# Kernel tuning notes

Hardware: AMD Instinct MI355X
Metric: run time of the kernel (lower is better)

## Reference

```python
import jax, jax.numpy as jnp
import numpy as np

NUM_LEVELS = 16
LEVEL_DIM = 2
BASE_RES = 16
MAX_RES = 2048
HASHMAP_SIZE = 1 << 19
N_POINTS = 2000000

# Instant-NGP geometric progression of grid resolutions
_scale = np.exp2(np.log2(MAX_RES / BASE_RES) / (NUM_LEVELS - 1))
RESOLUTIONS = [int(np.ceil(BASE_RES * _scale ** l)) for l in range(NUM_LEVELS)]

# corner offsets of the unit cube, shape [8, 3]
_OFFS = np.stack(np.meshgrid([0, 1], [0, 1], [0, 1], indexing='ij'), -1).reshape(8, 3)
_PRIMES = np.array([1, 2654435761, 805459861], dtype=np.uint32)


def grid_encode(x, table):
    """x: [N,3] in [0,1]; table: [L, T, F] -> [N, L*F]."""
    offs = jnp.asarray(_OFFS, dtype=jnp.int32)          # [8,3]
    feats = []
    for l, res in enumerate(RESOLUTIONS):
        pos = x * (res - 1)                              # [N,3]
        pos_i = jnp.clip(jnp.floor(pos).astype(jnp.int32), 0, res - 2)
        frac = pos - pos_i.astype(pos.dtype)             # [N,3]
        corners = pos_i[:, None, :] + offs[None]         # [N,8,3]
        if res ** 3 <= HASHMAP_SIZE:
            # dense (collision-free) indexing for coarse levels
            idx = corners[..., 0] + res * (corners[..., 1] + res * corners[..., 2])
        else:
            # spatial hash: xor of coordinate * prime, mod table size
            c = corners.astype(jnp.uint32)
            h = (c[..., 0] * _PRIMES[0]) ^ (c[..., 1] * _PRIMES[1]) ^ (c[..., 2] * _PRIMES[2])
            idx = (h % jnp.uint32(HASHMAP_SIZE)).astype(jnp.int32)
        vals = table[l][idx]                             # [N,8,F] gather
        # multilinear interpolation weights per corner
        w = jnp.prod(jnp.where(offs[None].astype(bool), frac[:, None, :], 1.0 - frac[:, None, :]), axis=-1)  # [N,8]
        feats.append(jnp.einsum('nc,ncf->nf', w, vals))
    return jnp.concatenate(feats, axis=-1)               # [N, 32]


def setup_inputs() -> dict:
    key = jax.random.key(0)
    ks = jax.random.split(key, 6)
    x = jax.random.uniform(ks[0], (N_POINTS, 3), dtype=jnp.float32)
    table = jax.random.uniform(ks[1], (NUM_LEVELS, HASHMAP_SIZE, LEVEL_DIM),
                               dtype=jnp.float32, minval=-1e-4, maxval=1e-4)
    in_dim = NUM_LEVELS * LEVEL_DIM  # 32
    W1 = jax.random.normal(ks[2], (in_dim, 64), dtype=jnp.float32) / np.sqrt(in_dim)
    W2 = jax.random.normal(ks[3], (64, 64), dtype=jnp.float32) / 8.0
    W3 = jax.random.normal(ks[4], (64, 64), dtype=jnp.float32) / 8.0
    Wo = jax.random.normal(ks[5], (64, 1), dtype=jnp.float32) / 8.0
    z = lambda n: jnp.zeros((n,), dtype=jnp.float32)
    return {"x": x, "table": table, "W1": W1, "b1": z(64), "W2": W2, "b2": z(64),
            "W3": W3, "b3": z(64), "Wo": Wo, "bo": z(1)}


def reference(x, table, W1, b1, W2, b2, W3, b3, Wo, bo):
    h = grid_encode(x, table)                 # [N,32]
    h = jax.nn.relu(h @ W1 + b1)
    h = jax.nn.relu(h @ W2 + b2)
    h = jax.nn.relu(h @ W3 + b3)
    return h @ Wo + bo                        # [N,1]
```

## Files before the change

### kernel.cpp

```cpp
#include <hip/hip_runtime.h>
#include <cmath>
#include <cstdint>


#define HASH_SZ (1u << 19)
#define HMASK   (HASH_SZ - 1u)
#define PR2 2654435761u
#define PR3 805459861u

typedef float v2f __attribute__((ext_vector_type(2)));
typedef float v4f __attribute__((ext_vector_type(4)));
typedef v4f v4fu __attribute__((aligned(8)));
typedef v2f v2fu __attribute__((aligned(8)));
typedef short bf16x8 __attribute__((ext_vector_type(8)));
typedef float f32x4 __attribute__((ext_vector_type(4)));

struct ResArr { int r[16]; };

__device__ __forceinline__ unsigned short bf16_rne(float f) {
    union { float f; unsigned u; } v; v.f = f;
    unsigned u = v.u;
    unsigned r = (u + 0x7fffu + ((u >> 16) & 1u)) >> 16;
    return (unsigned short)r;
}
__device__ __forceinline__ float bf16f(unsigned short h) {
    union { unsigned u; float f; } v; v.u = ((unsigned)h) << 16;
    return v.f;
}
__device__ __forceinline__ void split8(const float* x, bf16x8& hi, bf16x8& lo) {
    #pragma unroll
    for (int j = 0; j < 8; ++j) {
        union { float f; unsigned u; } v; v.f = x[j];
        const unsigned hu = v.u & 0xffff0000u;
        hi[j] = (short)(hu >> 16);
        union { unsigned u; float f; } hf; hf.u = hu;
        const float d = x[j] - hf.f;
        union { float f; unsigned u; } dv; dv.f = d;
        lo[j] = (short)((dv.u + 0x7fffu + ((dv.u >> 16) & 1u)) >> 16);
    }
}

__device__ __forceinline__ void gather_one(
    const v2f* __restrict__ tbl, int res, bool dense,
    float px, float py, float pz, float& A0, float& A1)
{
    const float rf = (float)(res - 1);
    const float fx = px * rf, fy = py * rf, fz = pz * rf;
    int ix = (int)floorf(fx), iy = (int)floorf(fy), iz = (int)floorf(fz);
    ix = min(max(ix, 0), res - 2);
    iy = min(max(iy, 0), res - 2);
    iz = min(max(iz, 0), res - 2);
    const float tx = fx - (float)ix, ty = fy - (float)iy, tz = fz - (float)iz;
    const float sx = 1.f - tx, sy = 1.f - ty, sz = 1.f - tz;
    float a0 = 0.f, a1 = 0.f;

    if (dense) {
        const int b0 = ix + res * (iy + res * iz);
        v4fu P[4];
        #pragma unroll
        for (int c = 0; c < 4; ++c) {
            const int dy = c >> 1, dz = c & 1;
            P[c] = *(const v4fu*)((const float*)tbl + 2 * (b0 + res * dy + res * res * dz));
        }
        #pragma unroll
        for (int c = 0; c < 4; ++c) {
            const int dy = c >> 1, dz = c & 1;
            const float wyz = (dy ? ty : sy) * (dz ? tz : sz);
            const float w0 = sx * wyz, w1 = tx * wyz;
            a0 = fmaf(w0, P[c].x, a0); a1 = fmaf(w0, P[c].y, a1);
            a0 = fmaf(w1, P[c].z, a0); a1 = fmaf(w1, P[c].w, a1);
        }
    } else {
        uint32_t i0[4], i1[4];
        v4f P[4];
        #pragma unroll
        for (int c = 0; c < 4; ++c) {
            const int dy = c >> 1, dz = c & 1;
            const uint32_t r = (uint32_t)(iy + dy) * PR2 ^ (uint32_t)(iz + dz) * PR3;
            i0[c] = ((uint32_t)ix ^ r) & HMASK;
            i1[c] = ((uint32_t)(ix + 1) ^ r) & HMASK;
            P[c] = *(const v4f*)((const float*)tbl + 2 * (i0[c] & ~1u));
        }
        const bool odd = (ix & 1);
        v2f O[4];
        if (odd) {
            #pragma unroll
            for (int c = 0; c < 4; ++c) O[c] = tbl[i1[c]];
        } else {
            #pragma unroll
            for (int c = 0; c < 4; ++c) { v2f z = {0.f, 0.f}; O[c] = z; }
        }
        #pragma unroll
        for (int c = 0; c < 4; ++c) {
            const int dy = c >> 1, dz = c & 1;
            const bool hi = (i0[c] & 1);
            v2f c0, e;
            c0.x = hi ? P[c].z : P[c].x;  c0.y = hi ? P[c].w : P[c].y;
            e.x  = hi ? P[c].x : P[c].z;  e.y  = hi ? P[c].y : P[c].w;
            const v2f c1 = odd ? O[c] : e;
            const float wyz = (dy ? ty : sy) * (dz ? tz : sz);
            const float w0 = sx * wyz, w1 = tx * wyz;
            a0 = fmaf(w0, c0.x, a0); a1 = fmaf(w0, c0.y, a1);
            a0 = fmaf(w1, c1.x, a0); a1 = fmaf(w1, c1.y, a1);
        }
    }
    A0 = a0; A1 = a1;
}

template<int NLEV>
__global__ __launch_bounds__(256, 8)
void encode_k(const float* __restrict__ x, const float* __restrict__ table,
              v2f* __restrict__ featT, int n, int lb, ResArr rv)
{
    const int nth2 = gridDim.x * 512;
    for (int q = (blockIdx.x * 256 + threadIdx.x) * 2; q < n; q += nth2) {
        float p0x, p0y, p0z, p1x, p1y, p1z;
        const bool two = (q + 1 < n);
        if (two) {
            const v4fu a = __builtin_nontemporal_load((const v4fu*)(x + 3 * q));
            const v2f  b = __builtin_nontemporal_load((const v2fu*)(x + 3 * q + 4));
            p0x = a.x; p0y = a.y; p0z = a.z; p1x = a.w; p1y = b.x; p1z = b.y;
        } else {
            p0x = x[3 * q]; p0y = x[3 * q + 1]; p0z = x[3 * q + 2];
            p1x = p0x; p1y = p0y; p1z = p0z;
        }
        #pragma unroll
        for (int il = 0; il < NLEV; ++il) {
            const int l = lb + il;
            const int res = rv.r[l];
            const bool dense = ((long long)res * res * res <= (long long)HASH_SZ);
            const v2f* tbl = (const v2f*)table + (size_t)l * HASH_SZ;
            float a00, a01, a10, a11;
            gather_one(tbl, res, dense, p0x, p0y, p0z, a00, a01);
            gather_one(tbl, res, dense, p1x, p1y, p1z, a10, a11);
            if (two) {
                v4f st; st.x = a00; st.y = a01; st.z = a10; st.w = a11;
                __builtin_nontemporal_store(st, (v4f*)&featT[(size_t)l * n + q]);
            } else {
                v2f st; st.x = a00; st.y = a01;
                __builtin_nontemporal_store(st, &featT[(size_t)l * n + q]);
            }
        }
    }
}

__global__ void prep_weights(const float* __restrict__ W1,
                             const float* __restrict__ W2,
                             const float* __restrict__ W3,
                             unsigned short* __restrict__ wb)
{
    const int tid = threadIdx.x;
    const int nb = tid >> 6, lane = tid & 63;
    const int l15 = lane & 15, q = lane >> 4;
    #pragma unroll
    for (int j = 0; j < 8; ++j) {
        const float v = W1[(q * 8 + j) * 64 + nb * 16 + l15];
        const unsigned short h = bf16_rne(v);
        wb[(nb * 64 + lane) * 8 + j] = h;
        wb[2048 + (nb * 64 + lane) * 8 + j] = bf16_rne(v - bf16f(h));
    }
    #pragma unroll
    for (int kb = 0; kb < 2; ++kb) {
        #pragma unroll
        for (int j = 0; j < 8; ++j) {
            const int row = kb * 32 + q * 8 + j;
            const int idx = ((kb * 4 + nb) * 64 + lane) * 8 + j;
            float v = W2[row * 64 + nb * 16 + l15];
            unsigned short h = bf16_rne(v);
            wb[4096 + idx] = h;
            wb[8192 + idx] = bf16_rne(v - bf16f(h));
            v = W3[row * 64 + nb * 16 + l15];
            h = bf16_rne(v);
            wb[12288 + idx] = h;
            wb[16384 + idx] = bf16_rne(v - bf16f(h));
        }
    }
}

#define TSTR 65

__global__ __launch_bounds__(256, 4)
void mlp_mfma(const v2f* __restrict__ featT,
              const unsigned short* __restrict__ wb,
              const float* __restrict__ b1, const float* __restrict__ b2,
              const float* __restrict__ b3,
              const float* __restrict__ Wo, const float* __restrict__ bo,
              float* __restrict__ out, int n)
{
    __shared__ float sact[4][32 * TSTR];
    const int wave = threadIdx.x >> 6;
    const int lane = threadIdx.x & 63;
    const int l15 = lane & 15, quad = lane >> 4;
    const int p0 = (blockIdx.x * 4 + wave) * 32;
    if (p0 >= n) return;

    bf16x8 ah[2], al[2];
    #pragma unroll
    for (int t = 0; t < 2; ++t) {
        const int p = p0 + t * 16 + l15;
        const int pl = (p < n) ? p : (n - 1);
        float xv[8];
        #pragma unroll
        for (int jj = 0; jj < 4; ++jj) {
            const v2f f = featT[(size_t)(quad * 4 + jj) * n + pl];
            xv[2 * jj] = f.x; xv[2 * jj + 1] = f.y;
        }
        split8(xv, ah[t], al[t]);
    }

    f32x4 acc[2][4];
    #pragma unroll
    for (int nb = 0; nb < 4; ++nb) {
        const bf16x8 wh = *(const bf16x8*)(wb + (nb * 64 + lane) * 8);
        const bf16x8 wl = *(const bf16x8*)(wb + 2048 + (nb * 64 + lane) * 8);
        const float bv = b1[nb * 16 + l15];
        #pragma unroll
        for (int t = 0; t < 2; ++t) {
            f32x4 c = {bv, bv, bv, bv};
            c = __builtin_amdgcn_mfma_f32_16x16x32_bf16(ah[t], wl, c, 0, 0, 0);
            c = __builtin_amdgcn_mfma_f32_16x16x32_bf16(al[t], wh, c, 0, 0, 0);
            c = __builtin_amdgcn_mfma_f32_16x16x32_bf16(ah[t], wh, c, 0, 0, 0);
            acc[t][nb] = c;
        }
    }

    #pragma unroll
    for (int layer = 0; layer < 2; ++layer) {
        #pragma unroll
        for (int t = 0; t < 2; ++t)
            #pragma unroll
            for (int nb = 0; nb < 4; ++nb)
                #pragma unroll
                for (int r = 0; r < 4; ++r)
                    sact[wave][(t * 16 + quad * 4 + r) * TSTR + nb * 16 + l15] =
                        fmaxf(acc[t][nb][r], 0.f);

        bf16x8 a2h[2][2], a2l[2][2];
        #pragma unroll
        for (int t = 0; t < 2; ++t) {
            float x2[16];
            #pragma unroll
            for (int kb = 0; kb < 2; ++kb)
                #pragma unroll
                for (int j = 0; j < 8; ++j)
                    x2[kb * 8 + j] =
                        sact[wave][(t * 16 + l15) * TSTR + kb * 32 + quad * 8 + j];
            split8(x2,     a2h[t][0], a2l[t][0]);
            split8(x2 + 8, a2h[t][1], a2l[t][1]);
        }

        const int base_h = layer ? 12288 : 4096;
        const int base_l = layer ? 16384 : 8192;
        const float* __restrict__ bias = layer ? b3 : b2;
        #pragma unroll
        for (int nb = 0; nb < 4; ++nb) {
            const float bv = bias[nb * 16 + l15];
            f32x4 c[2];
            #pragma unroll
            for (int t = 0; t < 2; ++t) { f32x4 z = {bv, bv, bv, bv}; c[t] = z; }
            #pragma unroll
            for (int kb = 0; kb < 2; ++kb) {
                const int idx = ((kb * 4 + nb) * 64 + lane) * 8;
                const bf16x8 wh = *(const bf16x8*)(wb + base_h + idx);
                const bf16x8 wl = *(const bf16x8*)(wb + base_l + idx);
                #pragma unroll
                for (int t = 0; t < 2; ++t) {
                    c[t] = __builtin_amdgcn_mfma_f32_16x16x32_bf16(a2h[t][kb], wl, c[t], 0, 0, 0);
                    c[t] = __builtin_amdgcn_mfma_f32_16x16x32_bf16(a2l[t][kb], wh, c[t], 0, 0, 0);
                    c[t] = __builtin_amdgcn_mfma_f32_16x16x32_bf16(a2h[t][kb], wh, c[t], 0, 0, 0);
                }
            }
            #pragma unroll
            for (int t = 0; t < 2; ++t) acc[t][nb] = c[t];
        }
    }

    const float wo = Wo[0 * 16 + l15];
    (void)wo;
    float part[2][4];
    #pragma unroll
    for (int t = 0; t < 2; ++t)
        #pragma unroll
        for (int r = 0; r < 4; ++r) {
            float s = 0.f;
            #pragma unroll
            for (int nb = 0; nb < 4; ++nb)
                s = fmaf(fmaxf(acc[t][nb][r], 0.f), Wo[nb * 16 + l15], s);
            part[t][r] = s;
        }
    #pragma unroll
    for (int mask = 1; mask < 16; mask <<= 1)
        #pragma unroll
        for (int t = 0; t < 2; ++t)
            #pragma unroll
            for (int r = 0; r < 4; ++r)
                part[t][r] += __shfl_xor(part[t][r], mask, 64);

    if (l15 == 0) {
        const float b = bo[0];
        #pragma unroll
        for (int t = 0; t < 2; ++t)
            #pragma unroll
            for (int r = 0; r < 4; ++r) {
                const int po = p0 + t * 16 + quad * 4 + r;
                if (po < n) out[po] = part[t][r] + b;
            }
    }
}

__global__ __launch_bounds__(256, 3)
void mlp_forward(const v2f* __restrict__ featT,
                 const float* __restrict__ W1, const float* __restrict__ b1,
                 const float* __restrict__ W2, const float* __restrict__ b2,
                 const float* __restrict__ W3, const float* __restrict__ b3,
                 const float* __restrict__ Wo, const float* __restrict__ bo,
                 float* __restrict__ out, int n)
{
    const int p = blockIdx.x * 256 + threadIdx.x;
    if (p >= n) return;
    const v2f z2 = {0.f, 0.f};
    v2f A[32], B[32];
    #pragma unroll
    for (int jq = 0; jq < 16; ++jq) {
        const v4f b = *(const v4f*)(b1 + 4 * jq);
        A[2 * jq] = b.xy; A[2 * jq + 1] = b.zw;
    }
    #pragma unroll
    for (int l = 0; l < 16; ++l) {
        const v2f f = __builtin_nontemporal_load(&featT[(size_t)l * n + p]);
        const v4f* w0 = (const v4f*)(W1 + (size_t)(2 * l) * 64);
        const v4f* w1 = (const v4f*)(W1 + (size_t)(2 * l + 1) * 64);
        const v2f h0 = {f.x, f.x}, h1 = {f.y, f.y};
        #pragma unroll
        for (int jq = 0; jq < 16; ++jq) {
            const v4f wa = w0[jq];
            A[2 * jq]     = __builtin_elementwise_fma(h0, wa.xy, A[2 * jq]);
            A[2 * jq + 1] = __builtin_elementwise_fma(h0, wa.zw, A[2 * jq + 1]);
        }
        #pragma unroll
        for (int jq = 0; jq < 16; ++jq) {
            const v4f wb2 = w1[jq];
            A[2 * jq]     = __builtin_elementwise_fma(h1, wb2.xy, A[2 * jq]);
            A[2 * jq + 1] = __builtin_elementwise_fma(h1, wb2.zw, A[2 * jq + 1]);
        }
    }
    #pragma unroll
    for (int j = 0; j < 32; ++j) A[j] = __builtin_elementwise_max(A[j], z2);
    #pragma unroll
    for (int jq = 0; jq < 16; ++jq) {
        const v4f b = *(const v4f*)(b2 + 4 * jq);
        B[2 * jq] = b.xy; B[2 * jq + 1] = b.zw;
    }
    #pragma unroll
    for (int k = 0; k < 64; ++k) {
        const float hv = A[k >> 1][k & 1];
        const v2f h = {hv, hv};
        const v4f* w = (const v4f*)(W2 + (size_t)k * 64);
        #pragma unroll
        for (int jq = 0; jq < 16; ++jq) {
            const v4f wa = w[jq];
            B[2 * jq]     = __builtin_elementwise_fma(h, wa.xy, B[2 * jq]);
            B[2 * jq + 1] = __builtin_elementwise_fma(h, wa.zw, B[2 * jq + 1]);
        }
    }
    #pragma unroll
    for (int j = 0; j < 32; ++j) B[j] = __builtin_elementwise_max(B[j], z2);
    #pragma unroll
    for (int jq = 0; jq < 16; ++jq) {
        const v4f b = *(const v4f*)(b3 + 4 * jq);
        A[2 * jq] = b.xy; A[2 * jq + 1] = b.zw;
    }
    #pragma unroll
    for (int k = 0; k < 64; ++k) {
        const float hv = B[k >> 1][k & 1];
        const v2f h = {hv, hv};
        const v4f* w = (const v4f*)(W3 + (size_t)k * 64);
        #pragma unroll
        for (int jq = 0; jq < 16; ++jq) {
            const v4f wa = w[jq];
            A[2 * jq]     = __builtin_elementwise_fma(h, wa.xy, A[2 * jq]);
            A[2 * jq + 1] = __builtin_elementwise_fma(h, wa.zw, A[2 * jq + 1]);
        }
    }
    v2f o2 = z2;
    #pragma unroll
    for (int jq = 0; jq < 16; ++jq) {
        const v4f wa = *(const v4f*)(Wo + 4 * jq);
        o2 = __builtin_elementwise_fma(__builtin_elementwise_max(A[2 * jq], z2),     wa.xy, o2);
        o2 = __builtin_elementwise_fma(__builtin_elementwise_max(A[2 * jq + 1], z2), wa.zw, o2);
    }
    out[p] = o2.x + o2.y + bo[0];
}

__global__ __launch_bounds__(256, 2)
void hashpinn_fused(const float* __restrict__ x,
                    const float* __restrict__ table,
                    const float* __restrict__ W1, const float* __restrict__ b1,
                    const float* __restrict__ W2, const float* __restrict__ b2,
                    const float* __restrict__ W3, const float* __restrict__ b3,
                    const float* __restrict__ Wo, const float* __restrict__ bo,
                    float* __restrict__ out, int n, ResArr rv)
{
    const int p = blockIdx.x * 256 + threadIdx.x;
    if (p >= n) return;
    const float px = x[3*p+0], py = x[3*p+1], pz = x[3*p+2];
    float feat[32];
    #pragma unroll
    for (int l = 0; l < 16; ++l) {
        const int res = rv.r[l];
        const float rf = (float)(res - 1);
        const float fx = px*rf, fy = py*rf, fz = pz*rf;
        int ix=(int)floorf(fx), iy=(int)floorf(fy), iz=(int)floorf(fz);
        ix=min(max(ix,0),res-2); iy=min(max(iy,0),res-2); iz=min(max(iz,0),res-2);
        const float tx=fx-(float)ix, ty=fy-(float)iy, tz=fz-(float)iz;
        const float sx=1.f-tx, sy=1.f-ty, sz=1.f-tz;
        const float2* tbl=(const float2*)table+(size_t)l*HASH_SZ;
        const bool dense=((long long)res*res*res<=(long long)HASH_SZ);
        float a0=0.f, a1=0.f;
        #pragma unroll
        for (int c=0;c<8;++c){
            const uint32_t cx=(uint32_t)(ix+((c>>2)&1));
            const uint32_t cy=(uint32_t)(iy+((c>>1)&1));
            const uint32_t cz=(uint32_t)(iz+(c&1));
            uint32_t idx = dense ? cx+(uint32_t)res*(cy+(uint32_t)res*cz)
                                 : ((cx*1u ^ cy*PR2 ^ cz*PR3)&HMASK);
            const float2 v=tbl[idx];
            const float w=(((c>>2)&1)?tx:sx)*(((c>>1)&1)?ty:sy)*((c&1)?tz:sz);
            a0=fmaf(w,v.x,a0); a1=fmaf(w,v.y,a1);
        }
        feat[2*l]=a0; feat[2*l+1]=a1;
    }
    float A[64], B[64];
    #pragma unroll
    for (int j=0;j<64;++j) A[j]=b1[j];
    #pragma unroll
    for (int k=0;k<32;++k){ const float h=feat[k];
        #pragma unroll
        for (int j=0;j<64;++j) A[j]=fmaf(h,W1[k*64+j],A[j]); }
    #pragma unroll 1
    for (int it=0;it<2;++it){
        const float* W = it?W3:W2; const float* bb = it?b3:b2;
        #pragma unroll
        for (int j=0;j<64;++j){ A[j]=fmaxf(A[j],0.f); B[j]=bb[j]; }
        #pragma unroll
        for (int k=0;k<64;++k){ const float h=A[k];
            #pragma unroll
            for (int j=0;j<64;++j) B[j]=fmaf(h,W[k*64+j],B[j]); }
        #pragma unroll
        for (int j=0;j<64;++j) A[j]=B[j];
    }
    float o=bo[0];
    #pragma unroll
    for (int j=0;j<64;++j) o=fmaf(fmaxf(A[j],0.f),Wo[j],o);
    out[p]=o;
}

static inline void launch_encode(int nlev, const float* x, const float* table,
                                 v2f* featT, int n, int lb, const ResArr& rv,
                                 hipStream_t stream) {
    const dim3 g(4096), b(256);
    switch (nlev) {
        case 1: hipLaunchKernelGGL(encode_k<1>, g, b, 0, stream, x, table, featT, n, lb, rv); break;
        case 2: hipLaunchKernelGGL(encode_k<2>, g, b, 0, stream, x, table, featT, n, lb, rv); break;
        case 3: hipLaunchKernelGGL(encode_k<3>, g, b, 0, stream, x, table, featT, n, lb, rv); break;
        case 4: hipLaunchKernelGGL(encode_k<4>, g, b, 0, stream, x, table, featT, n, lb, rv); break;
        case 5: hipLaunchKernelGGL(encode_k<5>, g, b, 0, stream, x, table, featT, n, lb, rv); break;
        case 6: hipLaunchKernelGGL(encode_k<6>, g, b, 0, stream, x, table, featT, n, lb, rv); break;
        case 7: hipLaunchKernelGGL(encode_k<7>, g, b, 0, stream, x, table, featT, n, lb, rv); break;
        default: hipLaunchKernelGGL(encode_k<8>, g, b, 0, stream, x, table, featT, n, lb, rv); break;
    }
}

extern "C" void kernel_launch(void* const* d_in, const int* in_sizes, int n_in,
                              void* d_out, int out_size, void* d_ws, size_t ws_size,
                              hipStream_t stream) {
    const float* x     = (const float*)d_in[0];
    const float* table = (const float*)d_in[1];
    const float* W1    = (const float*)d_in[2];
    const float* b1    = (const float*)d_in[3];
    const float* W2    = (const float*)d_in[4];
    const float* b2    = (const float*)d_in[5];
    const float* W3    = (const float*)d_in[6];
    const float* b3    = (const float*)d_in[7];
    const float* Wo    = (const float*)d_in[8];
    const float* bo    = (const float*)d_in[9];
    float* out = (float*)d_out;

    const int n = in_sizes[0] / 3;

    ResArr rv;
    const double scale = std::exp2(std::log2(2048.0 / 16.0) / 15.0);
    for (int l = 0; l < 16; ++l)
        rv.r[l] = (int)std::ceil(16.0 * std::pow(scale, (double)l));

    int dense_end = 0;
    while (dense_end < 16) {
        long long r = rv.r[dense_end];
        if (r * r * r <= (long long)HASH_SZ) ++dense_end; else break;
    }
    if (dense_end > 8) dense_end = 8;

    const size_t feat_bytes = (size_t)n * 16 * sizeof(v2f);
    const size_t wb_bytes = 20480 * sizeof(unsigned short);

    if (ws_size >= feat_bytes + wb_bytes) {
        v2f* featT = (v2f*)d_ws;
        unsigned short* wb = (unsigned short*)((char*)d_ws + feat_bytes);

        hipLaunchKernelGGL(prep_weights, dim3(1), dim3(256), 0, stream, W1, W2, W3, wb);

        if (dense_end > 0)
            launch_encode(dense_end, x, table, featT, n, 0, rv, stream);
        for (int l = dense_end; l < 16; ++l)
            launch_encode(1, x, table, featT, n, l, rv, stream);

        const int nblocks = (n + 127) / 128;
        hipLaunchKernelGGL(mlp_mfma, dim3(nblocks), dim3(256), 0, stream,
                           featT, wb, b1, b2, b3, Wo, bo, out, n);
    } else if (ws_size >= feat_bytes) {
        v2f* featT = (v2f*)d_ws;
        if (dense_end > 0)
            launch_encode(dense_end, x, table, featT, n, 0, rv, stream);
        for (int l = dense_end; l < 16; ++l)
            launch_encode(1, x, table, featT, n, l, rv, stream);
        hipLaunchKernelGGL(mlp_forward, dim3((n + 255) / 256), dim3(256), 0, stream,
                           featT, W1, b1, W2, b2, W3, b3, Wo, bo, out, n);
    } else {
        hipLaunchKernelGGL(hashpinn_fused, dim3((n + 255) / 256), dim3(256), 0, stream,
                           x, table, W1, b1, W2, b2, W3, b3, Wo, bo, out, n, rv);
    }
}
```

Before: 1.082 ms.

## Pre-split features to bf16 hi/lo in encoder and swap MLP activations via shuffles

The encoder now stores each feature pair as packed bf16 hi/lo words instead of fp32, so the MLP kernel loads ready-made MFMA operands without splitting them. The MFMA operand order is swapped (weights as A, activations as B), which lets inter-layer activations be redistributed with wave shuffles instead of a per-wave LDS transpose buffer. Bias and output-weight loads become vectorized, and the final reduction needs fewer shuffles. Dropping the LDS buffer allows a higher occupancy bound, at the cost of extra shuffle and select instructions and a fallback path that now decodes the packed format.

After: 1.133 ms. 1.05x slower.

```diff
diff --git a/kernel.cpp b/kernel.cpp
--- a/kernel.cpp
+++ b/kernel.cpp
@@ -14,6 +14,9 @@
 typedef v2f v2fu __attribute__((aligned(8)));
 typedef short bf16x8 __attribute__((ext_vector_type(8)));
 typedef float f32x4 __attribute__((ext_vector_type(4)));
+typedef unsigned int u32;
+typedef u32 u32x2 __attribute__((ext_vector_type(2)));
+typedef u32 u32x4 __attribute__((ext_vector_type(4)));
 
 struct ResArr { int r[16]; };
 
@@ -38,6 +41,19 @@
         union { float f; unsigned u; } dv; dv.f = d;
         lo[j] = (short)((dv.u + 0x7fffu + ((dv.u >> 16) & 1u)) >> 16);
     }
+}
+__device__ __forceinline__ u32 rne16u(float f) {
+    union { float f; u32 u; } v; v.f = f;
+    return (v.u + 0x7fffu + ((v.u >> 16) & 1u)) >> 16;
+}
+__device__ __forceinline__ u32x2 pack_split2(float f0, float f1) {
+    union { float f; u32 u; } a, b; a.f = f0; b.f = f1;
+    const u32 h0 = a.u & 0xffff0000u, h1 = b.u & 0xffff0000u;
+    union { u32 u; float f; } ha, hb; ha.u = h0; hb.u = h1;
+    u32x2 r;
+    r.x = (h0 >> 16) | h1;
+    r.y = rne16u(f0 - ha.f) | (rne16u(f1 - hb.f) << 16);
+    return r;
 }
 
 __device__ __forceinline__ void gather_one(
@@ -110,7 +126,7 @@
 template<int NLEV>
 __global__ __launch_bounds__(256, 8)
 void encode_k(const float* __restrict__ x, const float* __restrict__ table,
-              v2f* __restrict__ featT, int n, int lb, ResArr rv)
+              u32x2* __restrict__ featT, int n, int lb, ResArr rv)
 {
     const int nth2 = gridDim.x * 512;
     for (int q = (blockIdx.x * 256 + threadIdx.x) * 2; q < n; q += nth2) {
@@ -134,11 +150,13 @@
             gather_one(tbl, res, dense, p0x, p0y, p0z, a00, a01);
             gather_one(tbl, res, dense, p1x, p1y, p1z, a10, a11);
             if (two) {
-                v4f st; st.x = a00; st.y = a01; st.z = a10; st.w = a11;
-                __builtin_nontemporal_store(st, (v4f*)&featT[(size_t)l * n + q]);
+                const u32x2 e0 = pack_split2(a00, a01);
+                const u32x2 e1 = pack_split2(a10, a11);
+                u32x4 st; st.x = e0.x; st.y = e0.y; st.z = e1.x; st.w = e1.y;
+                __builtin_nontemporal_store(st, (u32x4*)&featT[(size_t)l * n + q]);
             } else {
-                v2f st; st.x = a00; st.y = a01;
-                __builtin_nontemporal_store(st, &featT[(size_t)l * n + q]);
+                __builtin_nontemporal_store(pack_split2(a00, a01),
+                                            &featT[(size_t)l * n + q]);
             }
         }
     }
@@ -177,35 +195,37 @@
     }
 }
 
-#define TSTR 65
-
-__global__ __launch_bounds__(256, 4)
-void mlp_mfma(const v2f* __restrict__ featT,
+__global__ __launch_bounds__(256, 6)
+void mlp_mfma(const u32x2* __restrict__ featT,
               const unsigned short* __restrict__ wb,
               const float* __restrict__ b1, const float* __restrict__ b2,
               const float* __restrict__ b3,
               const float* __restrict__ Wo, const float* __restrict__ bo,
               float* __restrict__ out, int n)
 {
-    __shared__ float sact[4][32 * TSTR];
     const int wave = threadIdx.x >> 6;
     const int lane = threadIdx.x & 63;
     const int l15 = lane & 15, quad = lane >> 4;
     const int p0 = (blockIdx.x * 4 + wave) * 32;
     if (p0 >= n) return;
 
-    bf16x8 ah[2], al[2];
+    const int s0 = (((2 * quad) & 3) << 4) + l15;
+    const int s1 = (((2 * quad + 1) & 3) << 4) + l15;
+    const bool hiHalf = (quad >= 2);
+
+    bf16x8 bh[2], bl[2];
     #pragma unroll
     for (int t = 0; t < 2; ++t) {
         const int p = p0 + t * 16 + l15;
         const int pl = (p < n) ? p : (n - 1);
-        float xv[8];
+        u32x4 hw, lw;
         #pragma unroll
         for (int jj = 0; jj < 4; ++jj) {
-            const v2f f = featT[(size_t)(quad * 4 + jj) * n + pl];
-            xv[2 * jj] = f.x; xv[2 * jj + 1] = f.y;
-        }
-        split8(xv, ah[t], al[t]);
+            const u32x2 v = featT[(size_t)(quad * 4 + jj) * n + pl];
+            hw[jj] = v.x; lw[jj] = v.y;
+        }
+        bh[t] = *(bf16x8*)&hw;
+        bl[t] = *(bf16x8*)&lw;
     }
 
     f32x4 acc[2][4];
@@ -213,51 +233,46 @@
     for (int nb = 0; nb < 4; ++nb) {
         const bf16x8 wh = *(const bf16x8*)(wb + (nb * 64 + lane) * 8);
         const bf16x8 wl = *(const bf16x8*)(wb + 2048 + (nb * 64 + lane) * 8);
-        const float bv = b1[nb * 16 + l15];
+        const f32x4 bv = *(const f32x4*)(b1 + nb * 16 + quad * 4);
         #pragma unroll
         for (int t = 0; t < 2; ++t) {
-            f32x4 c = {bv, bv, bv, bv};
-            c = __builtin_amdgcn_mfma_f32_16x16x32_bf16(ah[t], wl, c, 0, 0, 0);
-            c = __builtin_amdgcn_mfma_f32_16x16x32_bf16(al[t], wh, c, 0, 0, 0);
-            c = __builtin_amdgcn_mfma_f32_16x16x32_bf16(ah[t], wh, c, 0, 0, 0);
+            f32x4 c = bv;
+            c = __builtin_amdgcn_mfma_f32_16x16x32_bf16(wh, bl[t], c, 0, 0, 0);
+            c = __builtin_amdgcn_mfma_f32_16x16x32_bf16(wl, bh[t], c, 0, 0, 0);
+            c = __builtin_amdgcn_mfma_f32_16x16x32_bf16(wh, bh[t], c, 0, 0, 0);
             acc[t][nb] = c;
         }
     }
 
     #pragma unroll
     for (int layer = 0; layer < 2; ++layer) {
-        #pragma unroll
-        for (int t = 0; t < 2; ++t)
-            #pragma unroll
-            for (int nb = 0; nb < 4; ++nb)
+        bf16x8 nh[2][2], nl[2][2];
+        #pragma unroll
+        for (int t = 0; t < 2; ++t) {
+            #pragma unroll
+            for (int kb = 0; kb < 2; ++kb) {
+                float v[8];
                 #pragma unroll
-                for (int r = 0; r < 4; ++r)
-                    sact[wave][(t * 16 + quad * 4 + r) * TSTR + nb * 16 + l15] =
-                        fmaxf(acc[t][nb][r], 0.f);
-
-        bf16x8 a2h[2][2], a2l[2][2];
-        #pragma unroll
-        for (int t = 0; t < 2; ++t) {
-            float x2[16];
-            #pragma unroll
-            for (int kb = 0; kb < 2; ++kb)
-                #pragma unroll
-                for (int j = 0; j < 8; ++j)
-                    x2[kb * 8 + j] =
-                        sact[wave][(t * 16 + l15) * TSTR + kb * 32 + quad * 8 + j];
-            split8(x2,     a2h[t][0], a2l[t][0]);
-            split8(x2 + 8, a2h[t][1], a2l[t][1]);
-        }
-
+                for (int j = 0; j < 4; ++j) {
+                    const float a0 = __shfl(acc[t][2 * kb][j],     s0, 64);
+                    const float a1 = __shfl(acc[t][2 * kb + 1][j], s0, 64);
+                    const float c0 = __shfl(acc[t][2 * kb][j],     s1, 64);
+                    const float c1 = __shfl(acc[t][2 * kb + 1][j], s1, 64);
+                    v[j]     = fmaxf(hiHalf ? a1 : a0, 0.f);
+                    v[4 + j] = fmaxf(hiHalf ? c1 : c0, 0.f);
+                }
+                split8(v, nh[t][kb], nl[t][kb]);
+            }
+        }
         const int base_h = layer ? 12288 : 4096;
         const int base_l = layer ? 16384 : 8192;
         const float* __restrict__ bias = layer ? b3 : b2;
         #pragma unroll
         for (int nb = 0; nb < 4; ++nb) {
-            const float bv = bias[nb * 16 + l15];
+            const f32x4 bv = *(const f32x4*)(bias + nb * 16 + quad * 4);
             f32x4 c[2];
             #pragma unroll
-            for (int t = 0; t < 2; ++t) { f32x4 z = {bv, bv, bv, bv}; c[t] = z; }
+            for (int t = 0; t < 2; ++t) c[t] = bv;
             #pragma unroll
             for (int kb = 0; kb < 2; ++kb) {
                 const int idx = ((kb * 4 + nb) * 64 + lane) * 8;
@@ -265,9 +280,9 @@
                 const bf16x8 wl = *(const bf16x8*)(wb + base_l + idx);
                 #pragma unroll
                 for (int t = 0; t < 2; ++t) {
-                    c[t] = __builtin_amdgcn_mfma_f32_16x16x32_bf16(a2h[t][kb], wl, c[t], 0, 0, 0);
-                    c[t] = __builtin_amdgcn_mfma_f32_16x16x32_bf16(a2l[t][kb], wh, c[t], 0, 0, 0);
-                    c[t] = __builtin_amdgcn_mfma_f32_16x16x32_bf16(a2h[t][kb], wh, c[t], 0, 0, 0);
+                    c[t] = __builtin_amdgcn_mfma_f32_16x16x32_bf16(wh, nl[t][kb], c[t], 0, 0, 0);
+                    c[t] = __builtin_amdgcn_mfma_f32_16x16x32_bf16(wl, nh[t][kb], c[t], 0, 0, 0);
+                    c[t] = __builtin_amdgcn_mfma_f32_16x16x32_bf16(wh, nh[t][kb], c[t], 0, 0, 0);
                 }
             }
             #pragma unroll
@@ -275,41 +290,36 @@
         }
     }
 
-    const float wo = Wo[0 * 16 + l15];
-    (void)wo;
-    float part[2][4];
-    #pragma unroll
-    for (int t = 0; t < 2; ++t)
-        #pragma unroll
-        for (int r = 0; r < 4; ++r) {
-            float s = 0.f;
-            #pragma unroll
-            for (int nb = 0; nb < 4; ++nb)
-                s = fmaf(fmaxf(acc[t][nb][r], 0.f), Wo[nb * 16 + l15], s);
-            part[t][r] = s;
-        }
-    #pragma unroll
-    for (int mask = 1; mask < 16; mask <<= 1)
-        #pragma unroll
-        for (int t = 0; t < 2; ++t)
+    float part[2];
+    #pragma unroll
+    for (int t = 0; t < 2; ++t) {
+        float s = 0.f;
+        #pragma unroll
+        for (int nb = 0; nb < 4; ++nb) {
+            const f32x4 wo4 = *(const f32x4*)(Wo + nb * 16 + quad * 4);
             #pragma unroll
             for (int r = 0; r < 4; ++r)
-                part[t][r] += __shfl_xor(part[t][r], mask, 64);
-
-    if (l15 == 0) {
+                s = fmaf(fmaxf(acc[t][nb][r], 0.f), wo4[r], s);
+        }
+        part[t] = s;
+    }
+    #pragma unroll
+    for (int t = 0; t < 2; ++t) {
+        part[t] += __shfl_xor(part[t], 16, 64);
+        part[t] += __shfl_xor(part[t], 32, 64);
+    }
+    if (quad == 0) {
         const float b = bo[0];
         #pragma unroll
-        for (int t = 0; t < 2; ++t)
-            #pragma unroll
-            for (int r = 0; r < 4; ++r) {
-                const int po = p0 + t * 16 + quad * 4 + r;
-                if (po < n) out[po] = part[t][r] + b;
-            }
+        for (int t = 0; t < 2; ++t) {
+            const int po = p0 + t * 16 + l15;
+            if (po < n) out[po] = part[t] + b;
+        }
     }
 }
 
 __global__ __launch_bounds__(256, 3)
-void mlp_forward(const v2f* __restrict__ featT,
+void mlp_forward(const u32x2* __restrict__ featT,
                  const float* __restrict__ W1, const float* __restrict__ b1,
                  const float* __restrict__ W2, const float* __restrict__ b2,
                  const float* __restrict__ W3, const float* __restrict__ b3,
@@ -327,21 +337,25 @@
     }
     #pragma unroll
     for (int l = 0; l < 16; ++l) {
-        const v2f f = __builtin_nontemporal_load(&featT[(size_t)l * n + p]);
+        const u32x2 e = __builtin_nontemporal_load(&featT[(size_t)l * n + p]);
+        union { u32 u; float f; } h0, h1, l0, l1;
+        h0.u = e.x << 16; h1.u = e.x & 0xffff0000u;
+        l0.u = e.y << 16; l1.u = e.y & 0xffff0000u;
+        v2f f; f.x = h0.f + l0.f; f.y = h1.f + l1.f;
         const v4f* w0 = (const v4f*)(W1 + (size_t)(2 * l) * 64);
         const v4f* w1 = (const v4f*)(W1 + (size_t)(2 * l + 1) * 64);
-        const v2f h0 = {f.x, f.x}, h1 = {f.y, f.y};
+        const v2f hh0 = {f.x, f.x}, hh1 = {f.y, f.y};
         #pragma unroll
         for (int jq = 0; jq < 16; ++jq) {
             const v4f wa = w0[jq];
-            A[2 * jq]     = __builtin_elementwise_fma(h0, wa.xy, A[2 * jq]);
-            A[2 * jq + 1] = __builtin_elementwise_fma(h0, wa.zw, A[2 * jq + 1]);
+            A[2 * jq]     = __builtin_elementwise_fma(hh0, wa.xy, A[2 * jq]);
+            A[2 * jq + 1] = __builtin_elementwise_fma(hh0, wa.zw, A[2 * jq + 1]);
         }
         #pragma unroll
         for (int jq = 0; jq < 16; ++jq) {
             const v4f wb2 = w1[jq];
-            A[2 * jq]     = __builtin_elementwise_fma(h1, wb2.xy, A[2 * jq]);
-            A[2 * jq + 1] = __builtin_elementwise_fma(h1, wb2.zw, A[2 * jq + 1]);
+            A[2 * jq]     = __builtin_elementwise_fma(hh1, wb2.xy, A[2 * jq]);
+            A[2 * jq + 1] = __builtin_elementwise_fma(hh1, wb2.zw, A[2 * jq + 1]);
         }
     }
     #pragma unroll
@@ -456,7 +470,7 @@
 }
 
 static inline void launch_encode(int nlev, const float* x, const float* table,
-                                 v2f* featT, int n, int lb, const ResArr& rv,
+                                 u32x2* featT, int n, int lb, const ResArr& rv,
                                  hipStream_t stream) {
     const dim3 g(4096), b(256);
     switch (nlev) {
@@ -500,11 +514,11 @@
     }
     if (dense_end > 8) dense_end = 8;
 
-    const size_t feat_bytes = (size_t)n * 16 * sizeof(v2f);
+    const size_t feat_bytes = (size_t)n * 16 * sizeof(u32x2);
     const size_t wb_bytes = 20480 * sizeof(unsigned short);
 
     if (ws_size >= feat_bytes + wb_bytes) {
-        v2f* featT = (v2f*)d_ws;
+        u32x2* featT = (u32x2*)d_ws;
         unsigned short* wb = (unsigned short*)((char*)d_ws + feat_bytes);
 
         hipLaunchKernelGGL(prep_weights, dim3(1), dim3(256), 0, stream, W1, W2, W3, wb);
@@ -518,7 +532,7 @@
         hipLaunchKernelGGL(mlp_mfma, dim3(nblocks), dim3(256), 0, stream,
                            featT, wb, b1, b2, b3, Wo, bo, out, n);
     } else if (ws_size >= feat_bytes) {
-        v2f* featT = (v2f*)d_ws;
+        u32x2* featT = (u32x2*)d_ws;
         if (dense_end > 0)
             launch_encode(dense_end, x, table, featT, n, 0, rv, stream);
         for (int l = dense_end; l < 16; ++l)
```
